# Kernel optimization log

Measured on AMD Instinct MI355X. Metric: run time of the kernel, lower is better.

Reference implementation:

```python
import jax, jax.numpy as jnp
import numpy as np

N, E = 50000, 400000
N_INP, H, D = 256, 4, 32
HID = H * D
TN, TE, L, N_OUT = 4, 6, 2, 16
SQRT_D = float(np.sqrt(D))


def setup_inputs() -> dict:
    key = jax.random.key(0)
    ks = jax.random.split(key, 16)
    s = 0.05
    return {
        "x": jax.random.normal(ks[0], (N, N_INP), jnp.float32),
        "adapt_W": jax.random.normal(ks[1], (TN, N_INP, HID), jnp.float32) * s,
        "adapt_b": jnp.zeros((TN, HID), jnp.float32),
        "Wk": jax.random.normal(ks[2], (L, TN, HID, HID), jnp.float32) * s,
        "Wq": jax.random.normal(ks[3], (L, TN, HID, HID), jnp.float32) * s,
        "Wv": jax.random.normal(ks[4], (L, TN, HID, HID), jnp.float32) * s,
        "pri": jnp.ones((L, H, TE), jnp.float32),
        "Wa": jax.random.normal(ks[5], (L, H, TE, D, D), jnp.float32) * s,
        "Wm": jax.random.normal(ks[6], (L, H, TE, D, D), jnp.float32) * s,
        "Wla": jax.random.normal(ks[7], (L, TN, HID, HID), jnp.float32) * s,
        "skip": jnp.ones((L, TN), jnp.float32),
        "gamma": jnp.ones((L, HID), jnp.float32),
        "beta": jnp.zeros((L, HID), jnp.float32),
        "out_W": jax.random.normal(ks[8], (HID, N_OUT), jnp.float32) * s,
        "out_b": jnp.zeros((N_OUT,), jnp.float32),
        "ntype": jax.random.randint(ks[9], (N,), 0, TN),
        "etype": jax.random.randint(ks[10], (E,), 0, TE),
        "src": jax.random.randint(ks[11], (E,), 0, N),
        "dst": jax.random.randint(ks[12], (E,), 0, N),
    }


def typed_linear(x, W, types):
    # out[i] = x[i] @ W[types[i]]  (TypedLinear / per-type nn.Linear loop)
    out = jnp.zeros((x.shape[0], W.shape[-1]), x.dtype)
    for t in range(W.shape[0]):
        out = jnp.where((types == t)[:, None], x @ W[t], out)
    return out


def hgt_layer(h, ntype, etype, src, dst, Wk, Wq, Wv, pri, Wa, Wm, Wla, skip, gamma, beta):
    k = typed_linear(h, Wk, ntype).reshape(N, H, D)
    q = typed_linear(h, Wq, ntype).reshape(N, H, D)
    v = typed_linear(h, Wv, ntype).reshape(N, H, D)
    k_e, q_e, v_e = k[src], q[dst], v[src]  # [E,H,D] gathers
    a = jnp.zeros((E, H), h.dtype)
    m = jnp.zeros((E, H, D), h.dtype)
    for t in range(TE):  # small fixed loop over edge types (relation matrices)
        sel = etype == t
        kw = jnp.einsum('ehd,hdo->eho', k_e, Wa[:, t])
        sc = (kw * q_e).sum(-1) * pri[:, t][None, :] / SQRT_D  # [E,H]
        a = jnp.where(sel[:, None], sc, a)
        mt = jnp.einsum('ehd,hdo->eho', v_e, Wm[:, t])
        m = jnp.where(sel[:, None, None], mt, m)
    # edge softmax over incoming edges of each destination node
    amax = jax.ops.segment_max(a, dst, num_segments=N)
    ex = jnp.exp(a - amax[dst])
    den = jax.ops.segment_sum(ex, dst, num_segments=N)
    attn = ex / den[dst]
    agg = jax.ops.segment_sum(m * attn[:, :, None], dst, num_segments=N).reshape(N, HID)
    ha = typed_linear(agg, Wla, ntype)
    alpha = jax.nn.sigmoid(skip)[ntype][:, None]
    out = ha * alpha + h * (1.0 - alpha)
    mu = out.mean(-1, keepdims=True)
    var = jnp.mean((out - mu) ** 2, -1, keepdims=True)
    return (out - mu) / jnp.sqrt(var + 1e-5) * gamma + beta


def forward(x, adapt_W, adapt_b, Wk, Wq, Wv, pri, Wa, Wm, Wla, skip, gamma, beta, out_W, out_b, ntype, etype, src, dst):
    # per-node-type adapt linear + exact GELU
    h = typed_linear(x, adapt_W, ntype) + adapt_b[ntype]
    h = jax.nn.gelu(h, approximate=False)
    for l in range(L):
        h = hgt_layer(h, ntype, etype, src, dst, Wk[l], Wq[l], Wv[l], pri[l], Wa[l], Wm[l], Wla[l], skip[l], gamma[l], beta[l])
    return h @ out_W + out_b


def reference(x, adapt_W, adapt_b, Wk, Wq, Wv, pri, Wa, Wm, Wla, skip, gamma, beta, out_W, out_b, ntype, etype, src, dst):
    return forward(x, adapt_W, adapt_b, Wk, Wq, Wv, pri, Wa, Wm, Wla, skip, gamma, beta, out_W, out_b, ntype, etype, src, dst)
```

## Files before the change

### kernel.cpp

```cpp
#include <hip/hip_runtime.h>
#include <hip/hip_bf16.h>
#include <math.h>

#define NN   50000
#define EE   400000
#define NINP 256
#define HH   4
#define DD   32
#define HIDD 128
#define TNN  4
#define TEE  6
#define LLL  2
#define NOUTT 16
#define NB   196


typedef __attribute__((ext_vector_type(8))) short bf16x8;
typedef __attribute__((ext_vector_type(4))) float f32x4;

__device__ __forceinline__ float bf_lo(unsigned u) { return __uint_as_float(u << 16); }
__device__ __forceinline__ float bf_hi(unsigned u) { return __uint_as_float(u & 0xFFFF0000u); }
__device__ __forceinline__ unsigned f2bf(float f) {
    unsigned u = __float_as_uint(f);
    u += 0x7FFFu + ((u >> 16) & 1u);
    return (u >> 16);
}

__device__ __forceinline__ void gload_lds16(const unsigned short* g, unsigned short* l) {
    __builtin_amdgcn_global_load_lds(
        (__attribute__((address_space(1))) void*)(g),
        (__attribute__((address_space(3))) void*)(l), 16, 0, 0);
}

__global__ void k_init(int* __restrict__ deg, int* __restrict__ cur, int* __restrict__ ncnt,
                       int* __restrict__ ncur, int* __restrict__ nperm) {
    int i = blockIdx.x * 256 + threadIdx.x;
    if (i < NN) { deg[i] = 0; cur[i] = 0; }
    if (i < 16) { ncnt[i] = 0; ncur[i] = 0; }
    if (i < NN + 512) nperm[i] = -1;
}

__global__ void k_count_edges(const int* __restrict__ dst, int* __restrict__ deg) {
    int e = blockIdx.x * 256 + threadIdx.x;
    if (e < EE) atomicAdd(&deg[dst[e]], 1);
}
__global__ void k_count_types(const int* __restrict__ ntype, int* __restrict__ ncnt) {
    int n = blockIdx.x * 256 + threadIdx.x;
    int lane = threadIdx.x & 63;
    int t = (n < NN) ? ntype[n] : -1;
#pragma unroll
    for (int tt = 0; tt < TNN; tt++) {
        unsigned long long mask = __ballot(t == tt);
        if (mask && lane == (__ffsll((unsigned long long)mask) - 1))
            atomicAdd(&ncnt[tt], __popcll(mask));
    }
}
__global__ void k_scan1(const int* __restrict__ deg, int* __restrict__ bsum) {
    int i = blockIdx.x * 256 + threadIdx.x;
    int lane = threadIdx.x & 63, wv = threadIdx.x >> 6;
    __shared__ int ws[4];
    int x = (i < NN) ? deg[i] : 0;
#pragma unroll
    for (int off = 1; off < 64; off <<= 1) x += __shfl_xor(x, off);
    if (lane == 0) ws[wv] = x;
    __syncthreads();
    if (threadIdx.x == 0) bsum[blockIdx.x] = ws[0] + ws[1] + ws[2] + ws[3];
}
__global__ void k_scan2(const int* __restrict__ bsum, int* __restrict__ bpre,
                        const int* __restrict__ ncnt, int* __restrict__ meta) {
    __shared__ int ws[4];
    int tid = threadIdx.x, lane = tid & 63, wv = tid >> 6;
    int v = (tid < NB) ? bsum[tid] : 0;
    int x = v;
#pragma unroll
    for (int off = 1; off < 64; off <<= 1) {
        int y = __shfl_up(x, off);
        if (lane >= off) x += y;
    }
    if (lane == 63) ws[wv] = x;
    __syncthreads();
    if (tid == 0) { int a = 0; for (int w = 0; w < 4; w++) { int s = ws[w]; ws[w] = a; a += s; } }
    __syncthreads();
    if (tid < NB) bpre[tid] = x - v + ws[wv];
    if (tid == 0) {
        int acc = 0;
        meta[0] = 0;
        for (int t = 0; t < TNN; t++) { acc += ((ncnt[t] + 63) >> 6) << 6; meta[t + 1] = acc; }
    }
}
__global__ void k_scan3(const int* __restrict__ deg, const int* __restrict__ bpre,
                        int* __restrict__ offs) {
    int b = blockIdx.x;
    int tid = threadIdx.x, lane = tid & 63, wv = tid >> 6;
    int i = b * 256 + tid;
    __shared__ int ws[4];
    int v = (i < NN) ? deg[i] : 0;
    int x = v;
#pragma unroll
    for (int off = 1; off < 64; off <<= 1) {
        int y = __shfl_up(x, off);
        if (lane >= off) x += y;
    }
    if (lane == 63) ws[wv] = x;
    __syncthreads();
    if (tid == 0) { int a = 0; for (int w = 0; w < 4; w++) { int s = ws[w]; ws[w] = a; a += s; } }
    __syncthreads();
    if (i < NN) offs[i + 1] = x + ws[wv] + bpre[b];
    if (b == 0 && tid == 0) offs[0] = 0;
}
__global__ void k_scatter_edges(const int* __restrict__ dst, const int* __restrict__ src,
                                const int* __restrict__ etype, const int* __restrict__ offs,
                                int* __restrict__ cur, unsigned* __restrict__ se) {
    int e = blockIdx.x * 256 + threadIdx.x;
    if (e < EE) {
        int d = dst[e];
        int p = atomicAdd(&cur[d], 1);
        se[offs[d] + p] = ((unsigned)src[e] << 3) | (unsigned)etype[e];
    }
}
__global__ void k_scatter_nodes(const int* __restrict__ ntype, const int* __restrict__ meta,
                                int* __restrict__ ncur, int* __restrict__ nperm) {
    int n = blockIdx.x * 256 + threadIdx.x;
    int lane = threadIdx.x & 63;
    int t = (n < NN) ? ntype[n] : -1;
#pragma unroll
    for (int tt = 0; tt < TNN; tt++) {
        unsigned long long mask = __ballot(t == tt);
        if (t == tt) {
            int rank = __popcll(mask & ((1ull << lane) - 1ull));
            int leader = __ffsll((unsigned long long)mask) - 1;
            int b = 0;
            if (rank == 0) b = atomicAdd(&ncur[tt], __popcll(mask));
            b = __shfl(b, leader);
            nperm[meta[tt] + b + rank] = n;
        }
    }
}

__global__ void k_wt(const float* __restrict__ adapt_W, const float* __restrict__ Wk,
                     const float* __restrict__ Wla, unsigned short* __restrict__ adaptT,
                     unsigned short* __restrict__ Wf, unsigned short* __restrict__ WlaT) {
    __shared__ float Ts[64][68];
    int b = blockIdx.x, tid = threadIdx.x;
    const float* src;
    unsigned short* dst;
    int K, kt, nt, swz;
    if (b < 32) {
        int t = b >> 3, tile = b & 7;
        K = 256; kt = tile >> 1; nt = tile & 1; swz = 0;
        src = adapt_W + (size_t)t * 256 * 128;
        dst = adaptT + (size_t)t * 128 * 256;
    } else if (b < 64) {
        int b2 = b - 32, l = b2 >> 4, r = b2 & 15, t = r >> 2, tile = r & 3;
        K = 128; kt = tile >> 1; nt = tile & 1; swz = 1;
        src = Wk + (size_t)(l * 4 + t) * 16384;
        dst = Wf + (size_t)(l * TNN + t) * 1664 * 128;
    } else {
        int b2 = b - 64, l = b2 >> 4, r = b2 & 15, t = r >> 2, tile = r & 3;
        K = 128; kt = tile >> 1; nt = tile & 1; swz = 1;
        src = Wla + (size_t)(l * 4 + t) * 16384;
        dst = WlaT + (size_t)(l * 4 + t) * 16384;
    }
    int k0 = kt * 64, n0 = nt * 64;
#pragma unroll
    for (int it = 0; it < 4; it++) {
        int idx = tid + it * 256;
        int row = idx >> 4, c4 = (idx & 15) * 4;
        *(float4*)(&Ts[row][c4]) = *(const float4*)(src + (size_t)(k0 + row) * 128 + n0 + c4);
// ... 38 lines not shown
        *(float4*)(&Ls[kk][c4]) = *(const float4*)(L + (size_t)kk * 128 + hh * 32 + c4);
    }
    {
        int r = tid >> 3, c4 = (tid & 7) * 4;
        *(float4*)(&Ss[r][c4]) = *(const float4*)(S + r * 32 + c4);
    }
    __syncthreads();
    int k = tid >> 1, half = tid & 1;
#pragma unroll
    for (int jj = 0; jj < 16; jj++) {
        int j = half * 16 + jj;
        float s = 0.f;
        if (mode == 0) {
#pragma unroll
            for (int o = 0; o < 32; o++) s += Ls[k][o] * Ss[j][o];
        } else {
#pragma unroll
            for (int d = 0; d < 32; d++) s += Ls[k][d] * Ss[d][j];
        }
        Ot[j][k] = (unsigned short)f2bf(s * ps);
    }
    __syncthreads();
    unsigned short* dst = Wf + ((size_t)(l * TNN + t) * 1664 + (mode == 0 ? 128 : 896)) * 128;
#pragma unroll
    for (int it = 0; it < 2; it++) {
        int idx = tid + it * 256;
        int j = idx >> 4, sg = (idx & 15) * 8;
        uint4 pk = *(const uint4*)(&Ot[j][sg]);
        int jg = (hh * 6 + te) * 32 + j;
        *(uint4*)(dst + (size_t)jg * 128 + (sg ^ ((jg & 7) << 3))) = pk;
    }
}

template <int K, int NCB, int EPI, int OMODE, int AF32>
__launch_bounds__(256) __global__
void k_gemm(const void* __restrict__ Av, const unsigned short* __restrict__ WT,
            const float* __restrict__ bias, float* __restrict__ Yf,
            unsigned short* __restrict__ Yb, const int* __restrict__ nperm,
            const int* __restrict__ meta) {
    __shared__ __align__(16) char smem[52224];
    unsigned short* Ab = (unsigned short*)smem;
    unsigned short* Bs = (unsigned short*)(smem + 17408);
    float* Cb = (float*)(smem + 17408);
    const int WIDTH = NCB * 128;
    int row0 = blockIdx.x * 64;
    if (row0 >= meta[4]) return;
    int t = 0;
    while (t < 3 && row0 >= meta[t + 1]) t++;
    const unsigned short* WTt = WT + (size_t)t * WIDTH * K;
    int tid = threadIdx.x;
    int lane = tid & 63, w = tid >> 6;
    int m = lane & 15, q = lane >> 4;

#pragma unroll 1
    for (int cb = 0; cb < NCB; cb++) {
        f32x4 acc[4][2];
#pragma unroll
        for (int rt = 0; rt < 4; rt++)
#pragma unroll
            for (int ct = 0; ct < 2; ct++) acc[rt][ct] = (f32x4){0.f, 0.f, 0.f, 0.f};
#pragma unroll
        for (int kc = 0; kc < K / 128; kc++) {
            __syncthreads();
            if (AF32) {
                const float* A = (const float*)Av;
#pragma unroll
                for (int it = 0; it < 8; it++) {
                    int idx = tid + it * 256;
                    int r = idx >> 5, c4 = (idx & 31) * 4;
                    int node = nperm[row0 + r];
                    float4 v = make_float4(0.f, 0.f, 0.f, 0.f);
                    if (node >= 0)
                        v = *(const float4*)(A + (size_t)node * K + kc * 128 + c4);
                    uint2 pk;
                    pk.x = f2bf(v.x) | (f2bf(v.y) << 16);
                    pk.y = f2bf(v.z) | (f2bf(v.w) << 16);
                    *(uint2*)(Ab + r * 136 + c4) = pk;
                }
            }
#pragma unroll
            for (int it = 0; it < 8; it++) {
                int idx = tid + it * 256;
                int n = idx >> 4, sg = idx & 15;
                *(uint4*)(Bs + n * 136 + sg * 8) =
                    *(const uint4*)(WTt + (size_t)(cb * 128 + n) * K + kc * 128 + sg * 8);
            }
            __syncthreads();
#pragma unroll
            for (int k0 = 0; k0 < 128; k0 += 32) {
                bf16x8 b0 = *(const bf16x8*)(Bs + (w * 32 + m) * 136 + k0 + q * 8);
                bf16x8 b1 = *(const bf16x8*)(Bs + (w * 32 + 16 + m) * 136 + k0 + q * 8);
#pragma unroll
                for (int rt = 0; rt < 4; rt++) {
                    bf16x8 a = *(const bf16x8*)(Ab + (rt * 16 + m) * 136 + k0 + q * 8);
                    acc[rt][0] = __builtin_amdgcn_mfma_f32_16x16x32_bf16(a, b0, acc[rt][0], 0, 0, 0);
                    acc[rt][1] = __builtin_amdgcn_mfma_f32_16x16x32_bf16(a, b1, acc[rt][1], 0, 0, 0);
                }
            }
        }
#pragma unroll 1
        for (int hf = 0; hf < 2; hf++) {
            __syncthreads();
            if ((w >> 1) == hf) {
#pragma unroll
                for (int rt = 0; rt < 4; rt++)
#pragma unroll
                    for (int ct = 0; ct < 2; ct++)
#pragma unroll
                        for (int r = 0; r < 4; r++)
                            Cb[(rt * 16 + q * 4 + r) * 68 + (w & 1) * 32 + ct * 16 + m] =
                                acc[rt][ct][r];
            }
            __syncthreads();
#pragma unroll
            for (int it = 0; it < 4; it++) {
                int idx = tid + it * 256;
                int row = idx >> 4, c4 = (idx & 15) * 4;
                int node = nperm[row0 + row];
                if (node < 0) continue;
                float4 v = *(const float4*)(Cb + row * 68 + c4);
                if (EPI == 1) {
                    float4 bv = *(const float4*)(bias + t * 128 + hf * 64 + c4);
                    v.x += bv.x; v.y += bv.y; v.z += bv.z; v.w += bv.w;
                    const float is2 = 0.70710678118654752f;
                    v.x = 0.5f * v.x * (1.f + erff(v.x * is2));
                    v.y = 0.5f * v.y * (1.f + erff(v.y * is2));
                    v.z = 0.5f * v.z * (1.f + erff(v.z * is2));
                    v.w = 0.5f * v.w * (1.f + erff(v.w * is2));
                }
                int col = cb * 128 + hf * 64 + c4;
                if (OMODE == 0 || OMODE == 2)
                    *(float4*)(Yf + (size_t)node * WIDTH + col) = v;
                if (OMODE == 1 || OMODE == 2) {
                    uint2 pk;
                    pk.x = f2bf(v.x) | (f2bf(v.y) << 16);
                    pk.y = f2bf(v.z) | (f2bf(v.w) << 16);
                    *(uint2*)(Yb + (size_t)node * WIDTH + col) = pk;
                }
            }
        }
    }
}

template <int NCB, int EPI, int SPLIT>
__launch_bounds__(256) __global__
void k_gemm_reg(const unsigned short* __restrict__ A, const unsigned short* __restrict__ WT,
                unsigned short* __restrict__ Yb, const int* __restrict__ nperm,
                const int* __restrict__ meta, const float* __restrict__ skipv,
                const float* __restrict__ gamma, const float* __restrict__ beta,
                float* __restrict__ hres, unsigned short* __restrict__ hbout) {
    constexpr int SMEMB = (EPI == 2) ? 33792 : 32768;
    __shared__ __align__(16) char smem[SMEMB];
    unsigned short* Bs = (unsigned short*)smem;
    unsigned short* Cb16 = (unsigned short*)smem;
    float* Cbf = (float*)smem;
    const int WIDTH = NCB * 128;
    int tile = blockIdx.x / SPLIT;
    int par = blockIdx.x % SPLIT;
    int row0 = tile * 64;
    if (row0 >= meta[4]) return;
    int t = 0;
    while (t < 3 && row0 >= meta[t + 1]) t++;
    const unsigned short* WTt = WT + (size_t)t * WIDTH * 128;
    int tid = threadIdx.x;
    int lane = tid & 63, w = tid >> 6;
    int m = lane & 15, q = lane >> 4;

    bf16x8 a[4][4];
#pragma unroll
    for (int rt = 0; rt < 4; rt++) {
        int nd = nperm[row0 + rt * 16 + m];
#pragma unroll
        for (int kk = 0; kk < 4; kk++) {
            if (nd >= 0)
                a[rt][kk] = *(const bf16x8*)(A + (size_t)nd * 128 + kk * 32 + q * 8);
            else
                a[rt][kk] = (bf16x8){0, 0, 0, 0, 0, 0, 0, 0};
        }
    }

#pragma unroll 1
    for (int cb = par; cb < NCB; cb += SPLIT) {
        f32x4 acc[4][2];
#pragma unroll
        for (int rt = 0; rt < 4; rt++)
#pragma unroll
            for (int ct = 0; ct < 2; ct++) acc[rt][ct] = (f32x4){0.f, 0.f, 0.f, 0.f};
        __syncthreads();
        {
            const unsigned short* pan = WTt + (size_t)cb * 128 * 128;
#pragma unroll
            for (int it = 0; it < 8; it++) {
                int chunk = (it << 2) | w;
                gload_lds16(pan + chunk * 512 + lane * 8, Bs + chunk * 512);
            }
        }
        __syncthreads();
#pragma unroll
        for (int kk = 0; kk < 4; kk++) {
            int c = (kk * 32 + q * 8) ^ ((m & 7) << 3);
            bf16x8 b0 = *(const bf16x8*)(Bs + (w * 32 + m) * 128 + c);
            bf16x8 b1 = *(const bf16x8*)(Bs + (w * 32 + 16 + m) * 128 + c);
#pragma unroll
            for (int rt = 0; rt < 4; rt++) {
                acc[rt][0] = __builtin_amdgcn_mfma_f32_16x16x32_bf16(a[rt][kk], b0, acc[rt][0], 0, 0, 0);
                acc[rt][1] = __builtin_amdgcn_mfma_f32_16x16x32_bf16(a[rt][kk], b1, acc[rt][1], 0, 0, 0);
            }
        }
        __syncthreads();
        if (EPI == 2) {
#pragma unroll
            for (int rt = 0; rt < 4; rt++)
#pragma unroll
                for (int ct = 0; ct < 2; ct++)
#pragma unroll
                    for (int r = 0; r < 4; r++)
                        Cbf[(rt * 16 + q * 4 + r) * 132 + w * 32 + ct * 16 + m] = acc[rt][ct][r];
            __syncthreads();
            float alpha = 1.0f / (1.0f + __expf(-skipv[t]));
            int off = lane * 2;
            float2 g2 = *(const float2*)(gamma + off);
            float2 b2 = *(const float2*)(beta + off);
#pragma unroll 1
            for (int it = 0; it < 16; it++) {
                int row = w * 16 + it;
                int node = nperm[row0 + row];
                if (node < 0) continue;
                float ax = Cbf[row * 132 + off];
                float ay = Cbf[row * 132 + off + 1];
                float2 h2 = *(const float2*)(hres + (size_t)node * 128 + off);
                float ox = ax * alpha + h2.x * (1.f - alpha);
                float oy = ay * alpha + h2.y * (1.f - alpha);
                float s = ox + oy;
#pragma unroll
                for (int mm = 1; mm < 64; mm <<= 1) s += __shfl_xor(s, mm);
                float mu = s * (1.0f / 128.0f);
                float dx = ox - mu, dy = oy - mu;
                float v2 = dx * dx + dy * dy;
#pragma unroll
                for (int mm = 1; mm < 64; mm <<= 1) v2 += __shfl_xor(v2, mm);
                float rs = rsqrtf(v2 * (1.0f / 128.0f) + 1e-5f);
                float vx = dx * rs * g2.x + b2.x;
                float vy = dy * rs * g2.y + b2.y;
                *(float2*)(hres + (size_t)node * 128 + off) = make_float2(vx, vy);
                *(unsigned*)(hbout + (size_t)node * 128 + off) = f2bf(vx) | (f2bf(vy) << 16);
            }
        } else {
#pragma unroll
            for (int rt = 0; rt < 4; rt++)
#pragma unroll
                for (int ct = 0; ct < 2; ct++)
#pragma unroll
                    for (int r = 0; r < 4; r++)
                        Cb16[(rt * 16 + q * 4 + r) * 136 + w * 32 + ct * 16 + m] =
                            (unsigned short)f2bf(acc[rt][ct][r]);
            __syncthreads();
#pragma unroll
            for (int it = 0; it < 4; it++) {
                int idx = tid + it * 256;
                int row = idx >> 4, sg = idx & 15;
                int node = nperm[row0 + row];
                if (node < 0) continue;
                *(uint4*)(Yb + (size_t)node * WIDTH + cb * 128 + sg * 8) =
                    *(const uint4*)(Cb16 + row * 136 + sg * 8);
            }
        }
    }
}

__global__ void k_edge(const unsigned short* __restrict__ kqv,
                       const int* __restrict__ offs, const unsigned* __restrict__ se,
                       unsigned short* __restrict__ aggb) {
    int lane = threadIdx.x & 63;
    int wid = blockIdx.x * (blockDim.x >> 6) + (threadIdx.x >> 6);
    int nw = gridDim.x * (blockDim.x >> 6);
    int h = lane >> 4;
    int i2 = (lane & 15) * 2;
    int hoff = h * 32 + i2;
    for (int n = wid; n < NN; n += nw) {
        int e0 = offs[n], e1 = offs[n + 1];
        float ax = 0.f, ay = 0.f, den = 0.f;
        const unsigned short* qrow = kqv + (size_t)n * 1664 + 128;
        int s[4], t[4];
#pragma unroll
        for (int u = 0; u < 4; u++) {
            s[u] = 0; t[u] = 0;
            if (e0 + u < e1) { unsigned p0 = se[e0 + u]; s[u] = p0 >> 3; t[u] = p0 & 7; }
        }
        int j = e0;
        while (j + 3 < e1) {
            unsigned ku[4], qu[4], vu[4];
#pragma unroll
            for (int u = 0; u < 4; u++) {
                int to = (h * 6 + t[u]) * 32 + i2;
                ku[u] = *(const unsigned*)(kqv + (size_t)s[u] * 1664 + hoff);
                qu[u] = *(const unsigned*)(qrow + to);
                vu[u] = *(const unsigned*)(kqv + (size_t)s[u] * 1664 + 896 + to);
            }
            int jn = j + 4;
#pragma unroll
            for (int u = 0; u < 4; u++)
                if (jn + u < e1) { unsigned p0 = se[jn + u]; s[u] = p0 >> 3; t[u] = p0 & 7; }
            float p[4];
#pragma unroll
            for (int u = 0; u < 4; u++)
                p[u] = bf_lo(ku[u]) * bf_lo(qu[u]) + bf_hi(ku[u]) * bf_hi(qu[u]);
#pragma unroll
            for (int mm = 1; mm < 16; mm <<= 1) {
#pragma unroll
                for (int u = 0; u < 4; u++) p[u] += __shfl_xor(p[u], mm);
            }
#pragma unroll
            for (int u = 0; u < 4; u++) {
                float ex = __expf(p[u]);
                den += ex;
                ax += ex * bf_lo(vu[u]);
                ay += ex * bf_hi(vu[u]);
            }
            j = jn;
        }
        for (int u = 0; j < e1; j++, u++) {
            int to = (h * 6 + t[u]) * 32 + i2;
            unsigned ku = *(const unsigned*)(kqv + (size_t)s[u] * 1664 + hoff);
            unsigned qu = *(const unsigned*)(qrow + to);
            unsigned vu = *(const unsigned*)(kqv + (size_t)s[u] * 1664 + 896 + to);
            float p0 = bf_lo(ku) * bf_lo(qu) + bf_hi(ku) * bf_hi(qu);
            p0 += __shfl_xor(p0, 1);
            p0 += __shfl_xor(p0, 2);
            p0 += __shfl_xor(p0, 4);
            p0 += __shfl_xor(p0, 8);
            float ex = __expf(p0);
            den += ex;
            ax += ex * bf_lo(vu);
            ay += ex * bf_hi(vu);
        }
        float r = (den > 0.f) ? (1.0f / den) : 0.f;
        unsigned pk = f2bf(ax * r) | (f2bf(ay * r) << 16);
        *(unsigned*)(aggb + (size_t)n * 128 + hoff) = pk;
    }
}

__global__ void k_out(const unsigned short* __restrict__ hb, const float* __restrict__ Wo,
                      const float* __restrict__ bo, float* __restrict__ out) {
    __shared__ float Ws[128 * 16];
    int tid = threadIdx.x;
#pragma unroll
    for (int it = 0; it < 2; it++) {
        int idx = (tid + it * 256) * 4;
        *(float4*)(&Ws[idx]) = *(const float4*)(Wo + idx);
    }
    __syncthreads();
    int nl = tid >> 4;
    int o = tid & 15;
    int n = blockIdx.x * 16 + nl;
    float acc = bo[o];
    const unsigned short* hr = hb + (size_t)n * 128;
#pragma unroll
    for (int kk = 0; kk < 128; kk += 8) {
        uint4 hv = *(const uint4*)(hr + kk);
        acc += bf_lo(hv.x) * Ws[(kk + 0) * 16 + o] + bf_hi(hv.x) * Ws[(kk + 1) * 16 + o] +
               bf_lo(hv.y) * Ws[(kk + 2) * 16 + o] + bf_hi(hv.y) * Ws[(kk + 3) * 16 + o] +
               bf_lo(hv.z) * Ws[(kk + 4) * 16 + o] + bf_hi(hv.z) * Ws[(kk + 5) * 16 + o] +
               bf_lo(hv.w) * Ws[(kk + 6) * 16 + o] + bf_hi(hv.w) * Ws[(kk + 7) * 16 + o];
    }
    out[(size_t)n * 16 + o] = acc;
}

extern "C" void kernel_launch(void* const* d_in, const int* in_sizes, int n_in,
                              void* d_out, int out_size, void* d_ws, size_t ws_size,
                              hipStream_t stream) {
    const float* x       = (const float*)d_in[0];
    const float* adapt_W = (const float*)d_in[1];
    const float* adapt_b = (const float*)d_in[2];
    const float* Wk      = (const float*)d_in[3];
    const float* Wq      = (const float*)d_in[4];
    const float* Wv      = (const float*)d_in[5];
    const float* pri     = (const float*)d_in[6];
    const float* Wa      = (const float*)d_in[7];
    const float* Wm      = (const float*)d_in[8];
    const float* Wla     = (const float*)d_in[9];
    const float* skip    = (const float*)d_in[10];
    const float* gamma   = (const float*)d_in[11];
    const float* beta    = (const float*)d_in[12];
    const float* out_W   = (const float*)d_in[13];
    const float* out_b   = (const float*)d_in[14];
    const int* ntype     = (const int*)d_in[15];
    const int* etype     = (const int*)d_in[16];
    const int* src       = (const int*)d_in[17];
    const int* dst       = (const int*)d_in[18];
    float* out = (float*)d_out;

    char* p = (char*)d_ws;
    auto al = [](size_t v) { return (v + 255) & ~(size_t)255; };
    float* h  = (float*)p;          p += al((size_t)NN * 128 * 4);
    unsigned short* hb   = (unsigned short*)p; p += al((size_t)NN * 128 * 2);
    unsigned short* aggb = (unsigned short*)p; p += al((size_t)NN * 128 * 2);
    unsigned short* kqvb = (unsigned short*)p; p += al((size_t)NN * 1664 * 2);
    unsigned short* adaptT = (unsigned short*)p; p += al((size_t)TNN * 128 * 256 * 2);
    unsigned short* WlaT   = (unsigned short*)p; p += al((size_t)LLL * TNN * 16384 * 2);
    unsigned short* Wf     = (unsigned short*)p; p += al((size_t)LLL * TNN * 1664 * 128 * 2);
    int* deg   = (int*)p; p += al((size_t)NN * 4);
    int* offs  = (int*)p; p += al((size_t)(NN + 1) * 4);
    int* cur   = (int*)p; p += al((size_t)NN * 4);
    unsigned* se = (unsigned*)p; p += al((size_t)EE * 4);
    int* nperm = (int*)p; p += al((size_t)(NN + 512) * 4);
    int* bsum  = (int*)p; p += al(256 * 4);
    int* bpre  = (int*)p; p += al(256 * 4);
    int* ncnt  = (int*)p; p += al(64);
    int* ncur  = (int*)p; p += al(64);
    int* meta  = (int*)p; p += al(64);

    k_init<<<(NN + 512 + 255) / 256, 256, 0, stream>>>(deg, cur, ncnt, ncur, nperm);
    k_count_edges<<<(EE + 255) / 256, 256, 0, stream>>>(dst, deg);
    k_count_types<<<(NN + 255) / 256, 256, 0, stream>>>(ntype, ncnt);
    k_scan1<<<NB, 256, 0, stream>>>(deg, bsum);
    k_scan2<<<1, 256, 0, stream>>>(bsum, bpre, ncnt, meta);
    k_scan3<<<NB, 256, 0, stream>>>(deg, bpre, offs);
    k_scatter_edges<<<(EE + 255) / 256, 256, 0, stream>>>(dst, src, etype, offs, cur, se);
    k_scatter_nodes<<<(NN + 255) / 256, 256, 0, stream>>>(ntype, meta, ncur, nperm);

    k_wt<<<96, 256, 0, stream>>>(adapt_W, Wk, Wla, adaptT, Wf, WlaT);
    k_comb<<<384, 256, 0, stream>>>(Wq, Wa, Wv, Wm, pri, Wf);

    const int TILES = NN / 64 + TNN + 1;

    k_gemm<256, 1, 1, 2, 1><<<TILES, 256, 0, stream>>>(
        x, adaptT, adapt_b, h, hb, nperm, meta);

    for (int l = 0; l < LLL; l++) {
        k_gemm_reg<13, 0, 2><<<TILES * 2, 256, 0, stream>>>(
            hb, Wf + (size_t)l * TNN * 1664 * 128, kqvb, nperm, meta,
            nullptr, nullptr, nullptr, nullptr, nullptr);

        k_edge<<<4096, 256, 0, stream>>>(kqvb, offs, se, aggb);

        k_gemm_reg<1, 2, 1><<<TILES, 256, 0, stream>>>(
            aggb, WlaT + (size_t)l * TNN * 16384, nullptr, nperm, meta,
            skip + (size_t)l * TNN, gamma + (size_t)l * HIDD, beta + (size_t)l * HIDD,
            h, hb);
    }

    k_out<<<NN / 16, 256, 0, stream>>>(hb, out_W, out_b, out);
}
```

Measured before the change: 597.8 us.

## Split KQV projection GEMM into one workgroup per 64-row tile and column block

```diff
diff --git a/kernel.cpp b/kernel.cpp
--- a/kernel.cpp
+++ b/kernel.cpp
@@ -474,6 +474,92 @@
     }
 }
 
+template <int NCB>
+__launch_bounds__(256) __global__
+void k_kqv1(const unsigned short* __restrict__ A, const unsigned short* __restrict__ WT,
+            unsigned short* __restrict__ Yb, const int* __restrict__ nperm,
+            const int* __restrict__ meta) {
+    __shared__ __align__(16) char smem[32768];
+    unsigned short* Bs = (unsigned short*)smem;
+    unsigned short* Cb16 = (unsigned short*)smem;
+    const int WIDTH = NCB * 128;
+    int nwg = gridDim.x;
+    int bid = blockIdx.x;
+    int qx = nwg >> 3, rx = nwg & 7;
+    int xcd = bid & 7, pos = bid >> 3;
+    int logical = (xcd < rx ? xcd * (qx + 1) : rx * (qx + 1) + (xcd - rx) * qx) + pos;
+    int tile = logical / NCB;
+    int cb = logical - tile * NCB;
+    int row0 = tile * 64;
+    if (row0 >= meta[4]) return;
+    int t = 0;
+    while (t < 3 && row0 >= meta[t + 1]) t++;
+    const unsigned short* WTt = WT + (size_t)t * WIDTH * 128;
+    int tid = threadIdx.x;
+    int lane = tid & 63, w = tid >> 6;
+    int m = lane & 15, q = lane >> 4;
+
+    bf16x8 a[4][4];
+#pragma unroll
+    for (int rt = 0; rt < 4; rt++) {
+        int nd = nperm[row0 + rt * 16 + m];
+#pragma unroll
+        for (int kk = 0; kk < 4; kk++) {
+            if (nd >= 0)
+                a[rt][kk] = *(const bf16x8*)(A + (size_t)nd * 128 + kk * 32 + q * 8);
+            else
+                a[rt][kk] = (bf16x8){0, 0, 0, 0, 0, 0, 0, 0};
+        }
+    }
+
+    {
+        const unsigned short* pan = WTt + (size_t)cb * 128 * 128;
+#pragma unroll
+        for (int it = 0; it < 8; it++) {
+            int chunk = (it << 2) | w;
+            gload_lds16(pan + chunk * 512 + lane * 8, Bs + chunk * 512);
+        }
+    }
+    __syncthreads();
+
+    f32x4 acc[4][2];
+#pragma unroll
+    for (int rt = 0; rt < 4; rt++)
+#pragma unroll
+        for (int ct = 0; ct < 2; ct++) acc[rt][ct] = (f32x4){0.f, 0.f, 0.f, 0.f};
+#pragma unroll
+    for (int kk = 0; kk < 4; kk++) {
+        int c = (kk * 32 + q * 8) ^ ((m & 7) << 3);
+        bf16x8 b0 = *(const bf16x8*)(Bs + (w * 32 + m) * 128 + c);
+        bf16x8 b1 = *(const bf16x8*)(Bs + (w * 32 + 16 + m) * 128 + c);
+#pragma unroll
+        for (int rt = 0; rt < 4; rt++) {
+            acc[rt][0] = __builtin_amdgcn_mfma_f32_16x16x32_bf16(a[rt][kk], b0, acc[rt][0], 0, 0, 0);
+            acc[rt][1] = __builtin_amdgcn_mfma_f32_16x16x32_bf16(a[rt][kk], b1, acc[rt][1], 0, 0, 0);
+        }
+    }
+    __syncthreads();
+
+#pragma unroll
+    for (int rt = 0; rt < 4; rt++)
+#pragma unroll
+        for (int ct = 0; ct < 2; ct++)
+#pragma unroll
+            for (int r = 0; r < 4; r++)
+                Cb16[(rt * 16 + q * 4 + r) * 136 + w * 32 + ct * 16 + m] =
+                    (unsigned short)f2bf(acc[rt][ct][r]);
+    __syncthreads();
+#pragma unroll
+    for (int it = 0; it < 4; it++) {
+        int idx = tid + it * 256;
+        int row = idx >> 4, sg = idx & 15;
+        int node = nperm[row0 + row];
+        if (node < 0) continue;
+        *(uint4*)(Yb + (size_t)node * WIDTH + cb * 128 + sg * 8) =
+            *(const uint4*)(Cb16 + row * 136 + sg * 8);
+    }
+}
+
 __global__ void k_edge(const unsigned short* __restrict__ kqv,
                        const int* __restrict__ offs, const unsigned* __restrict__ se,
                        unsigned short* __restrict__ aggb) {
@@ -634,9 +720,8 @@
         x, adaptT, adapt_b, h, hb, nperm, meta);
 
     for (int l = 0; l < LLL; l++) {
-        k_gemm_reg<13, 0, 2><<<TILES * 2, 256, 0, stream>>>(
-            hb, Wf + (size_t)l * TNN * 1664 * 128, kqvb, nperm, meta,
-            nullptr, nullptr, nullptr, nullptr, nullptr);
+        k_kqv1<13><<<TILES * 13, 256, 0, stream>>>(
+            hb, Wf + (size_t)l * TNN * 1664 * 128, kqvb, nperm, meta);
 
         k_edge<<<4096, 256, 0, stream>>>(kqvb, offs, se, aggb);
 
```

Measured after the change: 668.4 us. +11.8%, slower.

## Keep node features in type-sorted order and store KQV as column planes

Applied to the files above, without the earlier changes.

```diff
diff --git a/kernel.cpp b/kernel.cpp
--- a/kernel.cpp
+++ b/kernel.cpp
@@ -2,17 +2,19 @@
 #include <hip/hip_bf16.h>
 #include <math.h>
 
-#define NN   50000
-#define EE   400000
-#define NINP 256
-#define HH   4
-#define DD   32
-#define HIDD 128
-#define TNN  4
-#define TEE  6
-#define LLL  2
+#define NN    50000
+#define EE    400000
+#define NINP  256
+#define HH    4
+#define DD    32
+#define HIDD  128
+#define TNN   4
+#define TEE   6
+#define LLL   2
 #define NOUTT 16
-#define NB   196
+#define TILES 786
+#define NROWS 50304
+#define NB2   197
 
 
 typedef __attribute__((ext_vector_type(8))) short bf16x8;
@@ -35,15 +37,10 @@
 __global__ void k_init(int* __restrict__ deg, int* __restrict__ cur, int* __restrict__ ncnt,
                        int* __restrict__ ncur, int* __restrict__ nperm) {
     int i = blockIdx.x * 256 + threadIdx.x;
-    if (i < NN) { deg[i] = 0; cur[i] = 0; }
+    if (i < NROWS) { deg[i] = 0; cur[i] = 0; nperm[i] = -1; }
     if (i < 16) { ncnt[i] = 0; ncur[i] = 0; }
-    if (i < NN + 512) nperm[i] = -1;
-}
-
-__global__ void k_count_edges(const int* __restrict__ dst, int* __restrict__ deg) {
-    int e = blockIdx.x * 256 + threadIdx.x;
-    if (e < EE) atomicAdd(&deg[dst[e]], 1);
-}
+}
+
 __global__ void k_count_types(const int* __restrict__ ntype, int* __restrict__ ncnt) {
     int n = blockIdx.x * 256 + threadIdx.x;
     int lane = threadIdx.x & 63;
@@ -55,71 +52,16 @@
             atomicAdd(&ncnt[tt], __popcll(mask));
     }
 }
-__global__ void k_scan1(const int* __restrict__ deg, int* __restrict__ bsum) {
-    int i = blockIdx.x * 256 + threadIdx.x;
-    int lane = threadIdx.x & 63, wv = threadIdx.x >> 6;
-    __shared__ int ws[4];
-    int x = (i < NN) ? deg[i] : 0;
-#pragma unroll
-    for (int off = 1; off < 64; off <<= 1) x += __shfl_xor(x, off);
-    if (lane == 0) ws[wv] = x;
-    __syncthreads();
-    if (threadIdx.x == 0) bsum[blockIdx.x] = ws[0] + ws[1] + ws[2] + ws[3];
-}
-__global__ void k_scan2(const int* __restrict__ bsum, int* __restrict__ bpre,
-                        const int* __restrict__ ncnt, int* __restrict__ meta) {
-    __shared__ int ws[4];
-    int tid = threadIdx.x, lane = tid & 63, wv = tid >> 6;
-    int v = (tid < NB) ? bsum[tid] : 0;
-    int x = v;
-#pragma unroll
-    for (int off = 1; off < 64; off <<= 1) {
-        int y = __shfl_up(x, off);
-        if (lane >= off) x += y;
-    }
-    if (lane == 63) ws[wv] = x;
-    __syncthreads();
-    if (tid == 0) { int a = 0; for (int w = 0; w < 4; w++) { int s = ws[w]; ws[w] = a; a += s; } }
-    __syncthreads();
-    if (tid < NB) bpre[tid] = x - v + ws[wv];
-    if (tid == 0) {
+__global__ void k_meta(const int* __restrict__ ncnt, int* __restrict__ meta) {
+    if (threadIdx.x == 0) {
         int acc = 0;
         meta[0] = 0;
         for (int t = 0; t < TNN; t++) { acc += ((ncnt[t] + 63) >> 6) << 6; meta[t + 1] = acc; }
     }
 }
-__global__ void k_scan3(const int* __restrict__ deg, const int* __restrict__ bpre,
-                        int* __restrict__ offs) {
-    int b = blockIdx.x;
-    int tid = threadIdx.x, lane = tid & 63, wv = tid >> 6;
-    int i = b * 256 + tid;
-    __shared__ int ws[4];
-    int v = (i < NN) ? deg[i] : 0;
-    int x = v;
-#pragma unroll
-    for (int off = 1; off < 64; off <<= 1) {
-        int y = __shfl_up(x, off);
-        if (lane >= off) x += y;
-    }
-    if (lane == 63) ws[wv] = x;
-    __syncthreads();
-    if (tid == 0) { int a = 0; for (int w = 0; w < 4; w++) { int s = ws[w]; ws[w] = a; a += s; } }
-    __syncthreads();
-    if (i < NN) offs[i + 1] = x + ws[wv] + bpre[b];
-    if (b == 0 && tid == 0) offs[0] = 0;
-}
-__global__ void k_scatter_edges(const int* __restrict__ dst, const int* __restrict__ src,
-                                const int* __restrict__ etype, const int* __restrict__ offs,
-                                int* __restrict__ cur, unsigned* __restrict__ se) {
-    int e = blockIdx.x * 256 + threadIdx.x;
-    if (e < EE) {
-        int d = dst[e];
-        int p = atomicAdd(&cur[d], 1);
-        se[offs[d] + p] = ((unsigned)src[e] << 3) | (unsigned)etype[e];
-    }
-}
 __global__ void k_scatter_nodes(const int* __restrict__ ntype, const int* __restrict__ meta,
-                                int* __restrict__ ncur, int* __restrict__ nperm) {
+                                int* __restrict__ ncur, int* __restrict__ nperm,
+                                int* __restrict__ iperm) {
     int n = blockIdx.x * 256 + threadIdx.x;
     int lane = threadIdx.x & 63;
     int t = (n < NN) ? ntype[n] : -1;
@@ -132,8 +74,74 @@
             int b = 0;
             if (rank == 0) b = atomicAdd(&ncur[tt], __popcll(mask));
             b = __shfl(b, leader);
-            nperm[meta[tt] + b + rank] = n;
-        }
+            int slot = meta[tt] + b + rank;
+            nperm[slot] = n;
+            iperm[n] = slot;
+        }
+    }
+}
+
+__global__ void k_count_edges(const int* __restrict__ dst, const int* __restrict__ iperm,
+                              int* __restrict__ deg) {
+    int e = blockIdx.x * 256 + threadIdx.x;
+    if (e < EE) atomicAdd(&deg[iperm[dst[e]]], 1);
+}
+__global__ void k_scan1(const int* __restrict__ deg, int* __restrict__ bsum) {
+    int i = blockIdx.x * 256 + threadIdx.x;
+    int lane = threadIdx.x & 63, wv = threadIdx.x >> 6;
+    __shared__ int ws[4];
+    int x = (i < NROWS) ? deg[i] : 0;
+#pragma unroll
+    for (int off = 1; off < 64; off <<= 1) x += __shfl_xor(x, off);
+    if (lane == 0) ws[wv] = x;
+    __syncthreads();
+    if (threadIdx.x == 0) bsum[blockIdx.x] = ws[0] + ws[1] + ws[2] + ws[3];
+}
+__global__ void k_scan2(const int* __restrict__ bsum, int* __restrict__ bpre) {
+    __shared__ int ws[4];
+    int tid = threadIdx.x, lane = tid & 63, wv = tid >> 6;
+    int v = (tid < NB2) ? bsum[tid] : 0;
+    int x = v;
+#pragma unroll
+    for (int off = 1; off < 64; off <<= 1) {
+        int y = __shfl_up(x, off);
+        if (lane >= off) x += y;
+    }
+    if (lane == 63) ws[wv] = x;
+    __syncthreads();
+    if (tid == 0) { int a = 0; for (int w = 0; w < 4; w++) { int s = ws[w]; ws[w] = a; a += s; } }
+    __syncthreads();
+    if (tid < NB2) bpre[tid] = x - v + ws[wv];
+}
+__global__ void k_scan3(const int* __restrict__ deg, const int* __restrict__ bpre,
+                        int* __restrict__ offs) {
+    int b = blockIdx.x;
+    int tid = threadIdx.x, lane = tid & 63, wv = tid >> 6;
+    int i = b * 256 + tid;
+    __shared__ int ws[4];
+    int v = (i < NROWS) ? deg[i] : 0;
+    int x = v;
+#pragma unroll
+    for (int off = 1; off < 64; off <<= 1) {
+        int y = __shfl_up(x, off);
+        if (lane >= off) x += y;
+    }
+    if (lane == 63) ws[wv] = x;
+    __syncthreads();
+    if (tid == 0) { int a = 0; for (int w = 0; w < 4; w++) { int s = ws[w]; ws[w] = a; a += s; } }
+    __syncthreads();
+    if (i < NROWS) offs[i + 1] = x + ws[wv] + bpre[b];
+    if (b == 0 && tid == 0) offs[0] = 0;
+}
+__global__ void k_scatter_edges(const int* __restrict__ dst, const int* __restrict__ src,
+                                const int* __restrict__ etype, const int* __restrict__ iperm,
+                                const int* __restrict__ offs, int* __restrict__ cur,
+                                unsigned* __restrict__ se) {
+    int e = blockIdx.x * 256 + threadIdx.x;
+    if (e < EE) {
+        int d = iperm[dst[e]];
+        int p = atomicAdd(&cur[d], 1);
+        se[offs[d] + p] = ((unsigned)iperm[src[e]] << 3) | (unsigned)etype[e];
     }
 }
 
@@ -238,9 +246,9 @@
     }
 }
 
-template <int K, int NCB, int EPI, int OMODE, int AF32>
+template <int K, int NCB>
 __launch_bounds__(256) __global__
-void k_gemm(const void* __restrict__ Av, const unsigned short* __restrict__ WT,
+void k_gemm(const float* __restrict__ A, const unsigned short* __restrict__ WT,
             const float* __restrict__ bias, float* __restrict__ Yf,
             unsigned short* __restrict__ Yb, const int* __restrict__ nperm,
             const int* __restrict__ meta) {
@@ -268,8 +276,7 @@
 #pragma unroll
         for (int kc = 0; kc < K / 128; kc++) {
             __syncthreads();
-            if (AF32) {
-                const float* A = (const float*)Av;
+            {
 #pragma unroll
                 for (int it = 0; it < 8; it++) {
                     int idx = tid + it * 256;
@@ -322,44 +329,124 @@
             for (int it = 0; it < 4; it++) {
                 int idx = tid + it * 256;
                 int row = idx >> 4, c4 = (idx & 15) * 4;
-                int node = nperm[row0 + row];
-                if (node < 0) continue;
                 float4 v = *(const float4*)(Cb + row * 68 + c4);
-                if (EPI == 1) {
-                    float4 bv = *(const float4*)(bias + t * 128 + hf * 64 + c4);
-                    v.x += bv.x; v.y += bv.y; v.z += bv.z; v.w += bv.w;
-                    const float is2 = 0.70710678118654752f;
-                    v.x = 0.5f * v.x * (1.f + erff(v.x * is2));
-                    v.y = 0.5f * v.y * (1.f + erff(v.y * is2));
-                    v.z = 0.5f * v.z * (1.f + erff(v.z * is2));
-                    v.w = 0.5f * v.w * (1.f + erff(v.w * is2));
-                }
+                float4 bv = *(const float4*)(bias + t * 128 + hf * 64 + c4);
+                v.x += bv.x; v.y += bv.y; v.z += bv.z; v.w += bv.w;
+                const float is2 = 0.70710678118654752f;
+                v.x = 0.5f * v.x * (1.f + erff(v.x * is2));
+                v.y = 0.5f * v.y * (1.f + erff(v.y * is2));
+                v.z = 0.5f * v.z * (1.f + erff(v.z * is2));
+                v.w = 0.5f * v.w * (1.f + erff(v.w * is2));
                 int col = cb * 128 + hf * 64 + c4;
-                if (OMODE == 0 || OMODE == 2)
-                    *(float4*)(Yf + (size_t)node * WIDTH + col) = v;
-                if (OMODE == 1 || OMODE == 2) {
-                    uint2 pk;
-                    pk.x = f2bf(v.x) | (f2bf(v.y) << 16);
-                    pk.y = f2bf(v.z) | (f2bf(v.w) << 16);
-                    *(uint2*)(Yb + (size_t)node * WIDTH + col) = pk;
-                }
-            }
-        }
-    }
-}
-
-template <int NCB, int EPI, int SPLIT>
+                *(float4*)(Yf + (size_t)(row0 + row) * WIDTH + col) = v;
+                uint2 pk;
+                pk.x = f2bf(v.x) | (f2bf(v.y) << 16);
+                pk.y = f2bf(v.z) | (f2bf(v.w) << 16);
+                *(uint2*)(Yb + (size_t)(row0 + row) * WIDTH + col) = pk;
+            }
+        }
+    }
+}
+
+template <int NCB>
 __launch_bounds__(256) __global__
 void k_gemm_reg(const unsigned short* __restrict__ A, const unsigned short* __restrict__ WT,
-                unsigned short* __restrict__ Yb, const int* __restrict__ nperm,
                 const int* __restrict__ meta, const float* __restrict__ skipv,
                 const float* __restrict__ gamma, const float* __restrict__ beta,
                 float* __restrict__ hres, unsigned short* __restrict__ hbout) {
-    constexpr int SMEMB = (EPI == 2) ? 33792 : 32768;
-    __shared__ __align__(16) char smem[SMEMB];
+    __shared__ __align__(16) char smem[33792];
+    unsigned short* Bs = (unsigned short*)smem;
+    float* Cbf = (float*)smem;
+    const int WIDTH = NCB * 128;
+    int row0 = blockIdx.x * 64;
+    if (row0 >= meta[4]) return;
+    int t = 0;
+    while (t < 3 && row0 >= meta[t + 1]) t++;
+    const unsigned short* WTt = WT + (size_t)t * WIDTH * 128;
+    int tid = threadIdx.x;
+    int lane = tid & 63, w = tid >> 6;
+    int m = lane & 15, q = lane >> 4;
+
+    bf16x8 a[4][4];
+#pragma unroll
+    for (int rt = 0; rt < 4; rt++)
+#pragma unroll
+        for (int kk = 0; kk < 4; kk++)
+            a[rt][kk] = *(const bf16x8*)(A + (size_t)(row0 + rt * 16 + m) * 128 + kk * 32 + q * 8);
+
+#pragma unroll 1
+    for (int cb = 0; cb < NCB; cb++) {
+        f32x4 acc[4][2];
+#pragma unroll
+        for (int rt = 0; rt < 4; rt++)
+#pragma unroll
+            for (int ct = 0; ct < 2; ct++) acc[rt][ct] = (f32x4){0.f, 0.f, 0.f, 0.f};
+        __syncthreads();
+        {
+            const unsigned short* pan = WTt + (size_t)cb * 128 * 128;
+#pragma unroll
+            for (int it = 0; it < 8; it++) {
+                int chunk = (it << 2) | w;
+                gload_lds16(pan + chunk * 512 + lane * 8, Bs + chunk * 512);
+            }
+        }
+        __syncthreads();
+#pragma unroll
+        for (int kk = 0; kk < 4; kk++) {
+            int c = (kk * 32 + q * 8) ^ ((m & 7) << 3);
+            bf16x8 b0 = *(const bf16x8*)(Bs + (w * 32 + m) * 128 + c);
+            bf16x8 b1 = *(const bf16x8*)(Bs + (w * 32 + 16 + m) * 128 + c);
+#pragma unroll
+            for (int rt = 0; rt < 4; rt++) {
+                acc[rt][0] = __builtin_amdgcn_mfma_f32_16x16x32_bf16(a[rt][kk], b0, acc[rt][0], 0, 0, 0);
+                acc[rt][1] = __builtin_amdgcn_mfma_f32_16x16x32_bf16(a[rt][kk], b1, acc[rt][1], 0, 0, 0);
+            }
+        }
+        __syncthreads();
+#pragma unroll
+        for (int rt = 0; rt < 4; rt++)
+#pragma unroll
+            for (int ct = 0; ct < 2; ct++)
+#pragma unroll
+                for (int r = 0; r < 4; r++)
+                    Cbf[(rt * 16 + q * 4 + r) * 132 + w * 32 + ct * 16 + m] = acc[rt][ct][r];
+        __syncthreads();
+        float alpha = 1.0f / (1.0f + __expf(-skipv[t]));
+        int off = lane * 2;
+        float2 g2 = *(const float2*)(gamma + off);
+        float2 b2 = *(const float2*)(beta + off);
+#pragma unroll 1
+        for (int it = 0; it < 16; it++) {
+            int row = w * 16 + it;
+            float ax = Cbf[row * 132 + off];
+            float ay = Cbf[row * 132 + off + 1];
+            float2 h2 = *(const float2*)(hres + (size_t)(row0 + row) * 128 + off);
+            float ox = ax * alpha + h2.x * (1.f - alpha);
+            float oy = ay * alpha + h2.y * (1.f - alpha);
+            float s = ox + oy;
+#pragma unroll
+            for (int mm = 1; mm < 64; mm <<= 1) s += __shfl_xor(s, mm);
+            float mu = s * (1.0f / 128.0f);
+            float dx = ox - mu, dy = oy - mu;
+            float v2 = dx * dx + dy * dy;
+#pragma unroll
+            for (int mm = 1; mm < 64; mm <<= 1) v2 += __shfl_xor(v2, mm);
+            float rs = rsqrtf(v2 * (1.0f / 128.0f) + 1e-5f);
+            float vx = dx * rs * g2.x + b2.x;
+            float vy = dy * rs * g2.y + b2.y;
+            *(float2*)(hres + (size_t)(row0 + row) * 128 + off) = make_float2(vx, vy);
+            *(unsigned*)(hbout + (size_t)(row0 + row) * 128 + off) = f2bf(vx) | (f2bf(vy) << 16);
+        }
+    }
+}
+
+template <int NCB, int SPLIT>
+__launch_bounds__(256) __global__
+void k_kqvP(const unsigned short* __restrict__ A, const unsigned short* __restrict__ WT,
+            unsigned short* __restrict__ Yb, const int* __restrict__ meta) {
+    __shared__ __align__(16) char smem[32768];
     unsigned short* Bs = (unsigned short*)smem;
     unsigned short* Cb16 = (unsigned short*)smem;
-    float* Cbf = (float*)smem;
     const int WIDTH = NCB * 128;
     int tile = blockIdx.x / SPLIT;
     int par = blockIdx.x % SPLIT;
@@ -374,16 +461,10 @@
 
     bf16x8 a[4][4];
 #pragma unroll
-    for (int rt = 0; rt < 4; rt++) {
-        int nd = nperm[row0 + rt * 16 + m];
-#pragma unroll
-        for (int kk = 0; kk < 4; kk++) {
-            if (nd >= 0)
-                a[rt][kk] = *(const bf16x8*)(A + (size_t)nd * 128 + kk * 32 + q * 8);
-            else
-                a[rt][kk] = (bf16x8){0, 0, 0, 0, 0, 0, 0, 0};
-        }
-    }
+    for (int rt = 0; rt < 4; rt++)
+#pragma unroll
+        for (int kk = 0; kk < 4; kk++)
+            a[rt][kk] = *(const bf16x8*)(A + (size_t)(row0 + rt * 16 + m) * 128 + kk * 32 + q * 8);
 
 #pragma unroll 1
     for (int cb = par; cb < NCB; cb += SPLIT) {
@@ -414,62 +495,21 @@
             }
         }
         __syncthreads();
-        if (EPI == 2) {
-#pragma unroll
-            for (int rt = 0; rt < 4; rt++)
-#pragma unroll
-                for (int ct = 0; ct < 2; ct++)
-#pragma unroll
-                    for (int r = 0; r < 4; r++)
-                        Cbf[(rt * 16 + q * 4 + r) * 132 + w * 32 + ct * 16 + m] = acc[rt][ct][r];
-            __syncthreads();
-            float alpha = 1.0f / (1.0f + __expf(-skipv[t]));
-            int off = lane * 2;
-            float2 g2 = *(const float2*)(gamma + off);
-            float2 b2 = *(const float2*)(beta + off);
-#pragma unroll 1
-            for (int it = 0; it < 16; it++) {
-                int row = w * 16 + it;
-                int node = nperm[row0 + row];
-                if (node < 0) continue;
-                float ax = Cbf[row * 132 + off];
-                float ay = Cbf[row * 132 + off + 1];
-                float2 h2 = *(const float2*)(hres + (size_t)node * 128 + off);
-                float ox = ax * alpha + h2.x * (1.f - alpha);
-                float oy = ay * alpha + h2.y * (1.f - alpha);
-                float s = ox + oy;
-#pragma unroll
-                for (int mm = 1; mm < 64; mm <<= 1) s += __shfl_xor(s, mm);
-                float mu = s * (1.0f / 128.0f);
-                float dx = ox - mu, dy = oy - mu;
-                float v2 = dx * dx + dy * dy;
-#pragma unroll
-                for (int mm = 1; mm < 64; mm <<= 1) v2 += __shfl_xor(v2, mm);
-                float rs = rsqrtf(v2 * (1.0f / 128.0f) + 1e-5f);
-                float vx = dx * rs * g2.x + b2.x;
-                float vy = dy * rs * g2.y + b2.y;
-                *(float2*)(hres + (size_t)node * 128 + off) = make_float2(vx, vy);
-                *(unsigned*)(hbout + (size_t)node * 128 + off) = f2bf(vx) | (f2bf(vy) << 16);
-            }
-        } else {
-#pragma unroll
-            for (int rt = 0; rt < 4; rt++)
-#pragma unroll
-                for (int ct = 0; ct < 2; ct++)
-#pragma unroll
-                    for (int r = 0; r < 4; r++)
-                        Cb16[(rt * 16 + q * 4 + r) * 136 + w * 32 + ct * 16 + m] =
-                            (unsigned short)f2bf(acc[rt][ct][r]);
-            __syncthreads();
-#pragma unroll
-            for (int it = 0; it < 4; it++) {
-                int idx = tid + it * 256;
-                int row = idx >> 4, sg = idx & 15;
-                int node = nperm[row0 + row];
-                if (node < 0) continue;
-                *(uint4*)(Yb + (size_t)node * WIDTH + cb * 128 + sg * 8) =
-                    *(const uint4*)(Cb16 + row * 136 + sg * 8);
-            }
+#pragma unroll
+        for (int rt = 0; rt < 4; rt++)
+#pragma unroll
+            for (int ct = 0; ct < 2; ct++)
+#pragma unroll
+                for (int r = 0; r < 4; r++)
+                    Cb16[(rt * 16 + q * 4 + r) * 136 + w * 32 + ct * 16 + m] =
+                        (unsigned short)f2bf(acc[rt][ct][r]);
+        __syncthreads();
+#pragma unroll
+        for (int it = 0; it < 4; it++) {
+            int idx = tid + it * 256;
+            int row = idx >> 4, sg = idx & 15;
+            *(uint4*)(Yb + ((size_t)cb * NROWS + row0 + row) * 128 + sg * 8) =
+                *(const uint4*)(Cb16 + row * 136 + sg * 8);
         }
     }
 }
@@ -477,16 +517,17 @@
 __global__ void k_edge(const unsigned short* __restrict__ kqv,
                        const int* __restrict__ offs, const unsigned* __restrict__ se,
                        unsigned short* __restrict__ aggb) {
+    const size_t PL = (size_t)NROWS * 128;
     int lane = threadIdx.x & 63;
     int wid = blockIdx.x * (blockDim.x >> 6) + (threadIdx.x >> 6);
     int nw = gridDim.x * (blockDim.x >> 6);
     int h = lane >> 4;
     int i2 = (lane & 15) * 2;
     int hoff = h * 32 + i2;
-    for (int n = wid; n < NN; n += nw) {
-        int e0 = offs[n], e1 = offs[n + 1];
+    int h6 = h * 6;
+    for (int r = wid; r < NROWS; r += nw) {
+        int e0 = offs[r], e1 = offs[r + 1];
         float ax = 0.f, ay = 0.f, den = 0.f;
-        const unsigned short* qrow = kqv + (size_t)n * 1664 + 128;
         int s[4], t[4];
 #pragma unroll
         for (int u = 0; u < 4; u++) {
@@ -498,10 +539,11 @@
             unsigned ku[4], qu[4], vu[4];
 #pragma unroll
             for (int u = 0; u < 4; u++) {
-                int to = (h * 6 + t[u]) * 32 + i2;
-                ku[u] = *(const unsigned*)(kqv + (size_t)s[u] * 1664 + hoff);
-                qu[u] = *(const unsigned*)(qrow + to);
-                vu[u] = *(const unsigned*)(kqv + (size_t)s[u] * 1664 + 896 + to);
+                int ht = h6 + t[u];
+                int cq = ((ht & 3) << 5) + i2;
+                ku[u] = *(const unsigned*)(kqv + (size_t)s[u] * 128 + hoff);
+                qu[u] = *(const unsigned*)(kqv + (size_t)(1 + (ht >> 2)) * PL + (size_t)r * 128 + cq);
+                vu[u] = *(const unsigned*)(kqv + (size_t)(7 + (ht >> 2)) * PL + (size_t)s[u] * 128 + cq);
             }
             int jn = j + 4;
 #pragma unroll
@@ -526,10 +568,11 @@
             j = jn;
         }
         for (int u = 0; j < e1; j++, u++) {
-            int to = (h * 6 + t[u]) * 32 + i2;
-            unsigned ku = *(const unsigned*)(kqv + (size_t)s[u] * 1664 + hoff);
-            unsigned qu = *(const unsigned*)(qrow + to);
-            unsigned vu = *(const unsigned*)(kqv + (size_t)s[u] * 1664 + 896 + to);
+            int ht = h6 + t[u];
+            int cq = ((ht & 3) << 5) + i2;
+            unsigned ku = *(const unsigned*)(kqv + (size_t)s[u] * 128 + hoff);
+            unsigned qu = *(const unsigned*)(kqv + (size_t)(1 + (ht >> 2)) * PL + (size_t)r * 128 + cq);
+            unsigned vu = *(const unsigned*)(kqv + (size_t)(7 + (ht >> 2)) * PL + (size_t)s[u] * 128 + cq);
             float p0 = bf_lo(ku) * bf_lo(qu) + bf_hi(ku) * bf_hi(qu);
             p0 += __shfl_xor(p0, 1);
             p0 += __shfl_xor(p0, 2);
@@ -540,14 +583,15 @@
             ax += ex * bf_lo(vu);
             ay += ex * bf_hi(vu);
         }
-        float r = (den > 0.f) ? (1.0f / den) : 0.f;
-        unsigned pk = f2bf(ax * r) | (f2bf(ay * r) << 16);
-        *(unsigned*)(aggb + (size_t)n * 128 + hoff) = pk;
+        float rr = (den > 0.f) ? (1.0f / den) : 0.f;
+        unsigned pk = f2bf(ax * rr) | (f2bf(ay * rr) << 16);
+        *(unsigned*)(aggb + (size_t)r * 128 + hoff) = pk;
     }
 }
 
 __global__ void k_out(const unsigned short* __restrict__ hb, const float* __restrict__ Wo,
-                      const float* __restrict__ bo, float* __restrict__ out) {
+                      const float* __restrict__ bo, float* __restrict__ out,
+                      const int* __restrict__ nperm) {
     __shared__ float Ws[128 * 16];
     int tid = threadIdx.x;
 #pragma unroll
@@ -558,9 +602,10 @@
     __syncthreads();
     int nl = tid >> 4;
     int o = tid & 15;
-    int n = blockIdx.x * 16 + nl;
+    int row = blockIdx.x * 16 + nl;
+    int node = nperm[row];
     float acc = bo[o];
-    const unsigned short* hr = hb + (size_t)n * 128;
+    const unsigned short* hr = hb + (size_t)row * 128;
 #pragma unroll
     for (int kk = 0; kk < 128; kk += 8) {
         uint4 hv = *(const uint4*)(hr + kk);
@@ -569,7 +614,7 @@
                bf_lo(hv.z) * Ws[(kk + 4) * 16 + o] + bf_hi(hv.z) * Ws[(kk + 5) * 16 + o] +
                bf_lo(hv.w) * Ws[(kk + 6) * 16 + o] + bf_hi(hv.w) * Ws[(kk + 7) * 16 + o];
     }
-    out[(size_t)n * 16 + o] = acc;
+    if (node >= 0) out[(size_t)node * 16 + o] = acc;
 }
 
 extern "C" void kernel_launch(void* const* d_in, const int* in_sizes, int n_in,
@@ -598,53 +643,52 @@
 
     char* p = (char*)d_ws;
     auto al = [](size_t v) { return (v + 255) & ~(size_t)255; };
-    float* h  = (float*)p;          p += al((size_t)NN * 128 * 4);
-    unsigned short* hb   = (unsigned short*)p; p += al((size_t)NN * 128 * 2);
-    unsigned short* aggb = (unsigned short*)p; p += al((size_t)NN * 128 * 2);
-    unsigned short* kqvb = (unsigned short*)p; p += al((size_t)NN * 1664 * 2);
+    float* h  = (float*)p;          p += al((size_t)NROWS * 128 * 4);
+    unsigned short* hb   = (unsigned short*)p; p += al((size_t)NROWS * 128 * 2);
+    unsigned short* aggb = (unsigned short*)p; p += al((size_t)NROWS * 128 * 2);
+    unsigned short* kqvb = (unsigned short*)p; p += al((size_t)NROWS * 1664 * 2);
     unsigned short* adaptT = (unsigned short*)p; p += al((size_t)TNN * 128 * 256 * 2);
     unsigned short* WlaT   = (unsigned short*)p; p += al((size_t)LLL * TNN * 16384 * 2);
     unsigned short* Wf     = (unsigned short*)p; p += al((size_t)LLL * TNN * 1664 * 128 * 2);
-    int* deg   = (int*)p; p += al((size_t)NN * 4);
-    int* offs  = (int*)p; p += al((size_t)(NN + 1) * 4);
-    int* cur   = (int*)p; p += al((size_t)NN * 4);
+    int* deg   = (int*)p; p += al((size_t)NROWS * 4);
+    int* offs  = (int*)p; p += al((size_t)(NROWS + 1) * 4);
+    int* cur   = (int*)p; p += al((size_t)NROWS * 4);
     unsigned* se = (unsigned*)p; p += al((size_t)EE * 4);
-    int* nperm = (int*)p; p += al((size_t)(NN + 512) * 4);
+    int* nperm = (int*)p; p += al((size_t)NROWS * 4);
+    int* iperm = (int*)p; p += al((size_t)NN * 4);
     int* bsum  = (int*)p; p += al(256 * 4);
     int* bpre  = (int*)p; p += al(256 * 4);
     int* ncnt  = (int*)p; p += al(64);
     int* ncur  = (int*)p; p += al(64);
     int* meta  = (int*)p; p += al(64);
 
-    k_init<<<(NN + 512 + 255) / 256, 256, 0, stream>>>(deg, cur, ncnt, ncur, nperm);
-    k_count_edges<<<(EE + 255) / 256, 256, 0, stream>>>(dst, deg);
+    k_init<<<NB2, 256, 0, stream>>>(deg, cur, ncnt, ncur, nperm);
     k_count_types<<<(NN + 255) / 256, 256, 0, stream>>>(ntype, ncnt);
-    k_scan1<<<NB, 256, 0, stream>>>(deg, bsum);
-    k_scan2<<<1, 256, 0, stream>>>(bsum, bpre, ncnt, meta);
-    k_scan3<<<NB, 256, 0, stream>>>(deg, bpre, offs);
-    k_scatter_edges<<<(EE + 255) / 256, 256, 0, stream>>>(dst, src, etype, offs, cur, se);
-    k_scatter_nodes<<<(NN + 255) / 256, 256, 0, stream>>>(ntype, meta, ncur, nperm);
+    k_meta<<<1, 64, 0, stream>>>(ncnt, meta);
+    k_scatter_nodes<<<(NN + 255) / 256, 256, 0, stream>>>(ntype, meta, ncur, nperm, iperm);
+    k_count_edges<<<(EE + 255) / 256, 256, 0, stream>>>(dst, iperm, deg);
+    k_scan1<<<NB2, 256, 0, stream>>>(deg, bsum);
+    k_scan2<<<1, 256, 0, stream>>>(bsum, bpre);
+    k_scan3<<<NB2, 256, 0, stream>>>(deg, bpre, offs);
+    k_scatter_edges<<<(EE + 255) / 256, 256, 0, stream>>>(dst, src, etype, iperm, offs, cur, se);
 
     k_wt<<<96, 256, 0, stream>>>(adapt_W, Wk, Wla, adaptT, Wf, WlaT);
     k_comb<<<384, 256, 0, stream>>>(Wq, Wa, Wv, Wm, pri, Wf);
 
-    const int TILES = NN / 64 + TNN + 1;
-
-    k_gemm<256, 1, 1, 2, 1><<<TILES, 256, 0, stream>>>(
+    k_gemm<256, 1><<<TILES, 256, 0, stream>>>(
         x, adaptT, adapt_b, h, hb, nperm, meta);
 
     for (int l = 0; l < LLL; l++) {
-        k_gemm_reg<13, 0, 2><<<TILES * 2, 256, 0, stream>>>(
-            hb, Wf + (size_t)l * TNN * 1664 * 128, kqvb, nperm, meta,
-            nullptr, nullptr, nullptr, nullptr, nullptr);
+        k_kqvP<13, 2><<<TILES * 2, 256, 0, stream>>>(
+            hb, Wf + (size_t)l * TNN * 1664 * 128, kqvb, meta);
 
         k_edge<<<4096, 256, 0, stream>>>(kqvb, offs, se, aggb);
 
-        k_gemm_reg<1, 2, 1><<<TILES, 256, 0, stream>>>(
-            aggb, WlaT + (size_t)l * TNN * 16384, nullptr, nperm, meta,
+        k_gemm_reg<1><<<TILES, 256, 0, stream>>>(
+            aggb, WlaT + (size_t)l * TNN * 16384, meta,
             skip + (size_t)l * TNN, gamma + (size_t)l * HIDD, beta + (size_t)l * HIDD,
             h, hb);
     }
 
-    k_out<<<NN / 16, 256, 0, stream>>>(hb, out_W, out_b, out);
-}
+    k_out<<<NROWS / 16, 256, 0, stream>>>(hb, out_W, out_b, out, nperm);
+}
```

After: 582.0 us. 2.6% less time.
